# Optimization experiments

Measured on AMD Instinct MI355X. Metric: run time of the kernel, lower is better.

The kernel has to match this reference:

```python
import jax, jax.numpy as jnp
import numpy as np

NC = 80          # num_classes
REG_MAX = 16
TOPK = 10
IMG = 640
STRIDES = (8, 16, 32)
EPS = 1e-9


def make_anchors(shapes, strides):
    pts, strs = [], []
    for (h, w), s in zip(shapes, strides):
        sx = jnp.arange(w, dtype=jnp.float32)  # grid_cell_offset = 0.0
        sy = jnp.arange(h, dtype=jnp.float32)
        gy, gx = jnp.meshgrid(sy, sx, indexing='ij')
        pts.append(jnp.stack([gx, gy], -1).reshape(-1, 2))
        strs.append(jnp.full((h * w, 1), float(s), dtype=jnp.float32))
    return jnp.concatenate(pts, 0), jnp.concatenate(strs, 0)  # [A,2], [A,1]


def ciou(box1, box2, eps=1e-7):
    # boxes are xyxy, broadcastable; returns CIoU with last dim squeezed
    b1x1, b1y1, b1x2, b1y2 = jnp.split(box1, 4, -1)
    b2x1, b2y1, b2x2, b2y2 = jnp.split(box2, 4, -1)
    w1, h1 = b1x2 - b1x1, b1y2 - b1y1
    w2, h2 = b2x2 - b2x1, b2y2 - b2y1
    inter = (jnp.clip(jnp.minimum(b1x2, b2x2) - jnp.maximum(b1x1, b2x1), 0.0)
             * jnp.clip(jnp.minimum(b1y2, b2y2) - jnp.maximum(b1y1, b2y1), 0.0))
    union = w1 * h1 + w2 * h2 - inter + eps
    iou = inter / union
    cw = jnp.maximum(b1x2, b2x2) - jnp.minimum(b1x1, b2x1)
    ch = jnp.maximum(b1y2, b2y2) - jnp.minimum(b1y1, b2y1)
    c2 = cw ** 2 + ch ** 2 + eps
    rho2 = ((b2x1 + b2x2 - b1x1 - b1x2) ** 2 + (b2y1 + b2y2 - b1y1 - b1y2) ** 2) / 4.0
    v = (4.0 / np.pi ** 2) * (jnp.arctan(w2 / (h2 + eps)) - jnp.arctan(w1 / (h1 + eps))) ** 2
    alpha = jax.lax.stop_gradient(v / (v - iou + (1.0 + eps)))
    return (iou - (rho2 / c2 + v * alpha))[..., 0]


def bbox_decode(anchor_points, pred_distri):
    # distribution-focal decode: softmax over REG_MAX bins, expectation, dist2bbox
    B, A, _ = pred_distri.shape
    pd = pred_distri.reshape(B, A, 4, REG_MAX)
    proj = jnp.arange(REG_MAX, dtype=jnp.float32)
    dist = jnp.einsum('bacr,r->bac', jax.nn.softmax(pd, -1), proj)  # [B,A,4] ltrb
    lt, rb = dist[..., :2], dist[..., 2:]
    return jnp.concatenate([anchor_points - lt, anchor_points + rb], -1)  # xyxy


def assigner(pd_scores, pd_bboxes, anc_points, gt_labels, gt_bboxes, mask_gt,
             alpha=0.5, beta=6.0):
    # pd_scores [B,A,C] (sigmoid), pd_bboxes [B,A,4], gt_* [B,M,...], mask_gt [B,M,1]
    B, A, C = pd_scores.shape
    M = gt_bboxes.shape[1]
    mask_gt = mask_gt.astype(jnp.float32)
    # anchors whose center lies inside each gt box
    lt = anc_points[None, None, :, :] - gt_bboxes[:, :, None, :2]   # [B,M,A,2]
    rb = gt_bboxes[:, :, None, 2:] - anc_points[None, None, :, :]
    mask_in_gts = (jnp.minimum(lt.min(-1), rb.min(-1)) > EPS).astype(jnp.float32)  # [B,M,A]
    mask = mask_in_gts * mask_gt
    # class score of each anchor at the gt's label
    sc = jnp.take_along_axis(pd_scores[:, None, :, :],
                             gt_labels[:, :, None, None].astype(jnp.int32), axis=-1)[..., 0]  # [B,M,A]
    overlaps = jnp.clip(ciou(gt_bboxes[:, :, None, :], pd_bboxes[:, None, :, :]), 0.0) * mask
    bbox_scores = sc * mask
    align_metric = (bbox_scores ** alpha) * (overlaps ** beta)  # [B,M,A]
    # top-k candidates per gt
    _, idxs = jax.lax.top_k(align_metric, TOPK)                 # [B,M,K]
    valid = jnp.broadcast_to(mask_gt > 0, (B, M, TOPK))
    idxs = jnp.where(valid, idxs, 0)
    cnt = jnp.zeros((B * M, A), jnp.float32).at[
        jnp.arange(B * M)[:, None], idxs.reshape(B * M, TOPK)
    ].add(valid.reshape(B * M, TOPK).astype(jnp.float32)).reshape(B, M, A)
    mask_topk = jnp.where(cnt > 1, 0.0, cnt)
    mask_pos = mask_topk * mask_in_gts * mask_gt               # [B,M,A]
    # resolve anchors assigned to multiple gts by max overlap
    fg = mask_pos.sum(1)                                       # [B,A]
    multi = fg[:, None, :] > 1
    is_max = jax.nn.one_hot(overlaps.argmax(1), M, dtype=jnp.float32).transpose(0, 2, 1)
    mask_pos = jnp.where(multi, is_max, mask_pos)
    fg_mask = mask_pos.sum(1)                                  # [B,A]
    tgt_idx = mask_pos.argmax(1)                               # [B,A]
    # gather targets
    flat = tgt_idx + jnp.arange(B)[:, None] * M
    t_labels = jnp.clip(gt_labels.reshape(-1)[flat], 0)        # [B,A]
    t_bboxes = gt_bboxes.reshape(-1, 4)[flat]                  # [B,A,4]
    t_scores = jax.nn.one_hot(t_labels, C, dtype=jnp.float32) * (fg_mask[..., None] > 0)
    # normalize scores by aligned metric
    am = align_metric * mask_pos
    pos_am = am.max(-1, keepdims=True)                         # [B,M,1]
    pos_ov = (overlaps * mask_pos).max(-1, keepdims=True)      # [B,M,1]
    norm = (am * pos_ov / (pos_am + EPS)).max(1)[..., None]    # [B,A,1]
    return t_bboxes, t_scores * norm, fg_mask > 0


def setup_inputs() -> dict:
    key = jax.random.key(0)
    ks = jax.random.split(key, 9)
    B, M = 16, 32
    inp = {
        'cls0': jax.random.normal(ks[0], (B, NC, 80, 80), jnp.float32),
        'cls1': jax.random.normal(ks[1], (B, NC, 40, 40), jnp.float32),
        'cls2': jax.random.normal(ks[2], (B, NC, 20, 20), jnp.float32),
        'reg0': jax.random.normal(ks[3], (B, 4 * REG_MAX, 80, 80), jnp.float32),
        'reg1': jax.random.normal(ks[4], (B, 4 * REG_MAX, 40, 40), jnp.float32),
        'reg2': jax.random.normal(ks[5], (B, 4 * REG_MAX, 20, 20), jnp.float32),
    }
    cxy = jax.random.uniform(ks[6], (B, M, 2), minval=0.1, maxval=0.9)
    wh = jax.random.uniform(ks[7], (B, M, 2), minval=0.02, maxval=0.25)
    inp['boxes'] = jnp.concatenate([cxy, wh], -1)  # normalized cxcywh
    inp['labels'] = jax.random.randint(ks[8], (B, M), 0, NC)
    return inp


def reference(cls0, cls1, cls2, reg0, reg1, reg2, boxes, labels):
    cls_out, reg_out = [cls0, cls1, cls2], [reg0, reg1, reg2]
    B = cls0.shape[0]
    anc, stride_t = make_anchors([r.shape[2:] for r in reg_out], STRIDES)
    pred_scores = jnp.concatenate(
        [c.transpose(0, 2, 3, 1).reshape(B, -1, NC) for c in cls_out], 1)        # [B,A,C]
    pred_distri = jnp.concatenate(
        [r.transpose(0, 2, 3, 1).reshape(B, -1, 4 * REG_MAX) for r in reg_out], 1)
    # gt2xyxy: normalized cxcywh -> pixel xyxy
    cx, cy, w, h = jnp.split(boxes, 4, -1)
    gt_bboxes = jnp.concatenate([(cx - w / 2) * IMG, (cy - h / 2) * IMG,
                                 (cx + w / 2) * IMG, (cy + h / 2) * IMG], -1)
    mask_gt = gt_bboxes.sum(2, keepdims=True) > 0.0
    pred_bboxes = bbox_decode(anc, pred_distri)                                   # anchor units
    sg = jax.lax.stop_gradient
    t_bboxes, t_scores, fg_mask = assigner(
        sg(jax.nn.sigmoid(pred_scores)), sg(pred_bboxes) * stride_t,
        anc * stride_t, labels, gt_bboxes, mask_gt)
    tss = jnp.maximum(t_scores.sum(), 1.0)
    # classification BCE-with-logits
    x, t = pred_scores, t_scores
    bce = jnp.maximum(x, 0.0) - x * t + jnp.log1p(jnp.exp(-jnp.abs(x)))
    l_cls = bce.sum() / tss
    # bbox CIoU loss
    t_bboxes = t_bboxes / stride_t
    weight = t_scores.sum(-1) * fg_mask                                           # [B,A]
    iou = ciou(pred_bboxes, t_bboxes)
    l_iou = ((1.0 - iou) * weight).sum() / tss
    # DFL loss
    tltrb = jnp.clip(jnp.concatenate([anc - t_bboxes[..., :2],
                                      t_bboxes[..., 2:] - anc], -1),
                     0.0, REG_MAX - 1 - 0.01)                                     # [B,A,4]
    logp = jax.nn.log_softmax(pred_distri.reshape(B, -1, 4, REG_MAX), -1)
    tl = jnp.floor(tltrb).astype(jnp.int32)
    wl = (tl + 1).astype(jnp.float32) - tltrb
    lp_tl = jnp.take_along_axis(logp, tl[..., None], -1)[..., 0]
    lp_tr = jnp.take_along_axis(logp, (tl + 1)[..., None], -1)[..., 0]
    dfl = (-(lp_tl * wl + lp_tr * (1.0 - wl))).mean(-1)                           # [B,A]
    l_dfl = (dfl * weight).sum() / tss
    loss = jnp.stack([0.5 * l_cls, 7.5 * l_iou, 1.5 * l_dfl])
    return loss.sum(), loss
```

## Files before the change

kernel.cpp:

```cpp
#include <hip/hip_runtime.h>

#define NB 16
#define NM 32
#define NA 8400
#define NCC 80
#define NREG 64
#define A0 6400
#define A1 1600
#define A2 400
#define CAP 768

#define TILES_PER_B 34
#define DEC_BLKS (NB * TILES_PER_B)
#define ASN_BLKS (NB * NM)
#define BCE_BLKS 2048
#define MID_GRID (ASN_BLKS + BCE_BLKS)
#define PL_GRID 525


__device__ __forceinline__ void anch(int a, float& ax, float& ay, float& s, int& lvl, int& p) {
  if (a < A0)            { lvl = 0; p = a;          s = 8.f;  ax = (float)(p % 80); ay = (float)(p / 80); }
  else if (a < A0 + A1)  { lvl = 1; p = a - A0;     s = 16.f; ax = (float)(p % 40); ay = (float)(p / 40); }
  else                   { lvl = 2; p = a - A0 - A1; s = 32.f; ax = (float)(p % 20); ay = (float)(p / 20); }
}

__device__ __forceinline__ float cls_at(const float* c0, const float* c1, const float* c2,
                                        int b, int ch, int a) {
  if (a < A0)           return c0[((size_t)(b * NCC + ch)) * A0 + a];
  if (a < A0 + A1)      return c1[((size_t)(b * NCC + ch)) * A1 + (a - A0)];
  return c2[((size_t)(b * NCC + ch)) * A2 + (a - A0 - A1)];
}

__device__ __forceinline__ float reg_at(const float* r0, const float* r1, const float* r2,
                                        int b, int ch, int lvl, int p) {
  if (lvl == 0) return r0[((size_t)(b * NREG + ch)) * A0 + p];
  if (lvl == 1) return r1[((size_t)(b * NREG + ch)) * A1 + p];
  return r2[((size_t)(b * NREG + ch)) * A2 + p];
}

__device__ __forceinline__ void gtbox(const float* boxes, int b, int m,
                                      float& x1, float& y1, float& x2, float& y2, bool& valid) {
  const float* q = boxes + ((size_t)(b * NM + m)) * 4;
  float cx = q[0], cy = q[1], w = q[2], h = q[3];
  x1 = (cx - w * 0.5f) * 640.f; y1 = (cy - h * 0.5f) * 640.f;
  x2 = (cx + w * 0.5f) * 640.f; y2 = (cy + h * 0.5f) * 640.f;
  valid = (x1 + y1 + x2 + y2) > 0.f;
}

__device__ __forceinline__ float ciou_f(float b1x1, float b1y1, float b1x2, float b1y2,
                                        float b2x1, float b2y1, float b2x2, float b2y2) {
  const float eps = 1e-7f;
  float w1 = b1x2 - b1x1, h1 = b1y2 - b1y1;
  float w2 = b2x2 - b2x1, h2 = b2y2 - b2y1;
  float iw = fmaxf(fminf(b1x2, b2x2) - fmaxf(b1x1, b2x1), 0.f);
  float ih = fmaxf(fminf(b1y2, b2y2) - fmaxf(b1y1, b2y1), 0.f);
  float inter = iw * ih;
  float uni = w1 * h1 + w2 * h2 - inter + eps;
  float iou = inter / uni;
  float cw = fmaxf(b1x2, b2x2) - fminf(b1x1, b2x1);
  float ch = fmaxf(b1y2, b2y2) - fminf(b1y1, b2y1);
  float c2 = cw * cw + ch * ch + eps;
  float dx = b2x1 + b2x2 - b1x1 - b1x2;
  float dy = b2y1 + b2y2 - b1y1 - b1y2;
  float rho2 = (dx * dx + dy * dy) * 0.25f;
  float at = atanf(w2 / (h2 + eps)) - atanf(w1 / (h1 + eps));
  float v = 0.4052847345693511f * at * at;
  float alpha = v / (v - iou + (1.0f + eps));
  return iou - (rho2 / c2 + v * alpha);
}

__device__ __forceinline__ float align_of(float sc, float o) {
  float o2 = o * o, o4 = o2 * o2;
  return sqrtf(sc) * (o2 * o4);
}

__device__ __forceinline__ float softplus_fast(float x) {
  float e = __expf(-fabsf(x));
  return fmaxf(x, 0.f) + __logf(1.f + e);
}


__global__ __launch_bounds__(256) void k_dec(
    const float* r0, const float* r1, const float* r2,
    float4* bb4, float4* mls4, int* fgcnt, int* msum,
    unsigned* pos_am, unsigned* pos_ov, double* gt_acc, int* done_ctr) {
  __shared__ float lds[32 * 256];
  const int tid = threadIdx.x;
  const int g = blockIdx.x * 256 + tid;
  if (g < NB * NA) { fgcnt[g] = 0; msum[g] = 0; }
  if (g < NB * NM) { pos_am[g] = 0u; pos_ov[g] = 0u; }
  if (g < NB * NM * 4) gt_acc[g] = 0.0;
  if (g == 0) *done_ctr = 0;

  const int d = blockIdx.x;
  const int b = d / TILES_PER_B, u = d % TILES_PER_B;
  int lvl, tile;
  if (u < 25)      { lvl = 0; tile = u; }
  else if (u < 32) { lvl = 1; tile = u - 25; }
  else             { lvl = 2; tile = u - 32; }
  const int HW   = (lvl == 0) ? A0 : (lvl == 1 ? A1 : A2);
  const int W    = (lvl == 0) ? 80 : (lvl == 1 ? 40 : 20);
  const int loff = (lvl == 0) ? 0  : (lvl == 1 ? A0 : A0 + A1);
  const float* rg = (lvl == 0) ? r0 : (lvl == 1 ? r1 : r2);
  const int base_p = tile * 256;
  const int valid  = min(256, HW - base_p);
  const float* src = rg + (size_t)b * NREG * HW + base_p;

  float dist[4], mlv[4];
#pragma unroll
  for (int ph = 0; ph < 2; ++ph) {
    for (int ch = 0; ch < 32; ++ch) {
      if (tid < valid)
        lds[ch * 256 + tid] = src[(size_t)(ph * 32 + ch) * HW + tid];
    }
    __syncthreads();
    if (tid < valid) {
#pragma unroll
      for (int sh = 0; sh < 2; ++sh) {
        const float* col = &lds[(sh * 16) * 256 + tid];
        float mx = col[0];
#pragma unroll
        for (int r = 1; r < 16; ++r) mx = fmaxf(mx, col[r * 256]);
        float se = 0.f, ws = 0.f;
#pragma unroll
        for (int r = 0; r < 16; ++r) {
          float e = __expf(col[r * 256] - mx);
          se += e; ws += e * (float)r;
        }
        dist[ph * 2 + sh] = ws / se;
        mlv[ph * 2 + sh]  = mx + __logf(se);
      }
    }
    __syncthreads();
  }
  if (tid < valid) {
    int p = base_p + tid;
    float ax = (float)(p % W), ay = (float)(p / W);
    int t = b * NA + loff + p;
    bb4[t]  = make_float4(ax - dist[0], ay - dist[1], ax + dist[2], ay + dist[3]);
    mls4[t] = make_float4(mlv[0], mlv[1], mlv[2], mlv[3]);
  }
}


__global__ __launch_bounds__(256) void k_mid(
    const float* boxes, const int* labels, const float4* bb,
    const float* c0, const float* c1, const float* c2,
    int* fgcnt, int* msum, double* bce_part) {
  __shared__ float sv[CAP];
  __shared__ int   si[CAP];
  __shared__ int   s_n;
  __shared__ double sred[256];
  const int tid = threadIdx.x;

  if (blockIdx.x >= ASN_BLKS) {
    const int bce_blk = blockIdx.x - ASN_BLKS;
    const size_t N0 = (size_t)NB * NCC * A0 / 4;
    const size_t N1 = (size_t)NB * NCC * A1 / 4;
    const size_t N2 = (size_t)NB * NCC * A2 / 4;
    const size_t NT = N0 + N1 + N2;
    const float4* f0 = (const float4*)c0;
    const float4* f1 = (const float4*)c1;
    const float4* f2 = (const float4*)c2;
    const size_t i0 = (size_t)bce_blk * 256 + tid;
    const size_t stride = (size_t)BCE_BLKS * 256;
    float s0 = 0.f, s1 = 0.f;
    for (size_t i = i0; i < NT; i += stride) {
      float4 v;
      if (i < N0) v = f0[i];
      else if (i < N0 + N1) v = f1[i - N0];
      else v = f2[i - N0 - N1];
      s0 += softplus_fast(v.x) + softplus_fast(v.z);
      s1 += softplus_fast(v.y) + softplus_fast(v.w);
    }
    sred[tid] = (double)(s0 + s1);
    __syncthreads();
    for (int off = 128; off; off >>= 1) {
      if (tid < off) sred[tid] += sred[tid + off];
      __syncthreads();
    }
    if (tid == 0) bce_part[bce_blk] = sred[0];
    return;
  }

  const int bm = blockIdx.x;
  const int b = bm / NM, m = bm % NM;
  const int lane = tid & 63;

  float gx1, gy1, gx2, gy2; bool valid;
  gtbox(boxes, b, m, gx1, gy1, gx2, gy2, valid);
  if (!valid) return;
  int lbl = labels[bm]; if (lbl < 0) lbl = 0; if (lbl >= NCC) lbl = NCC - 1;
  if (tid == 0) s_n = 0;
  __syncthreads();

  const int   Ws[3]   = {80, 40, 20};
  const float ss[3]   = {8.f, 16.f, 32.f};
  const int   loff[3] = {0, A0, A0 + A1};
  int rx0[3], ry0[3], rw[3], bc[3];
  int total = 0;
  for (int l = 0; l < 3; ++l) {
    float s = ss[l]; int W = Ws[l];
    int ax0 = (int)floorf((gx1 + 1e-9f) / s);
    int ax1 = (int)ceilf((gx2 - 1e-9f) / s);
    int ay0 = (int)floorf((gy1 + 1e-9f) / s);
    int ay1 = (int)ceilf((gy2 - 1e-9f) / s);
    ax0 = max(ax0, 0); ay0 = max(ay0, 0);
    ax1 = min(ax1, W - 1); ay1 = min(ay1, W - 1);
    rx0[l] = ax0; ry0[l] = ay0;
    rw[l] = max(0, ax1 - ax0 + 1);
    int rhl = max(0, ay1 - ay0 + 1);
    bc[l] = total;
    total += rw[l] * rhl;
  }
  int iters = (total + 255) >> 8;
  for (int it = 0; it < iters; ++it) {
    int idx = it * 256 + tid;
    bool pred = false; float am = 0.f; int a = 0;
    if (idx < total) {
      int l = (idx >= bc[2]) ? 2 : ((idx >= bc[1]) ? 1 : 0);
      int r = idx - bc[l];
      int iy = r / rw[l], ix = r - iy * rw[l];
      int axg = rx0[l] + ix, ayg = ry0[l] + iy;
      a = loff[l] + ayg * Ws[l] + axg;
      float s = ss[l];
      float axp = (float)axg * s, ayp = (float)ayg * s;
      float mn = fminf(fminf(axp - gx1, ayp - gy1), fminf(gx2 - axp, gy2 - ayp));
      if (mn > 1e-9f) {
        pred = true;
        float4 pb = bb[(size_t)b * NA + a];
        float c = ciou_f(gx1, gy1, gx2, gy2, pb.x * s, pb.y * s, pb.z * s, pb.w * s);
        float o = fmaxf(c, 0.f);
        float x = cls_at(c0, c1, c2, b, lbl, a);
        float sc = 1.f / (1.f + expf(-x));
        am = align_of(sc, o);
      }
    }
    unsigned long long mask = __ballot(pred);
    if (mask) {
      int nact = __popcll(mask);
      int leader = __ffsll(mask) - 1;
      int basec = 0;
      if (lane == leader) basec = atomicAdd(&s_n, nact);
      basec = __shfl(basec, leader);
      if (pred) {
        int off = basec + __popcll(mask & ((1ull << lane) - 1ull));
        if (off < CAP) { sv[off] = am; si[off] = a; }
      }
    }
  }
  __syncthreads();
  int n = s_n; if (n > CAP) n = CAP;
  if (n == 0) return;
  if (tid >= 64) return;

  float v[12]; int ix[12];
#pragma unroll
  for (int k = 0; k < 12; ++k) {
    int j = k * 64 + tid;
    bool in = (j < n);
    v[k]  = in ? sv[j] : -2.f;
    ix[k] = in ? si[j] : (1 << 30);
  }
  int cnt = 0;
#pragma unroll
  for (int k = 0; k < 12; ++k) cnt += (v[k] > 0.f) ? 1 : 0;
  for (int o = 32; o; o >>= 1) cnt += __shfl_xor(cnt, o);
  int npos = cnt;

  if (npos > 10) {
    for (int p = 0; p < 10; ++p) {
      float bv = -1.f; int bi = 1 << 30;
#pragma unroll
      for (int k = 0; k < 12; ++k) {
        if (v[k] > bv || (v[k] == bv && ix[k] < bi)) { bv = v[k]; bi = ix[k]; }
      }
      for (int o = 32; o; o >>= 1) {
        float wv = __shfl_xor(bv, o); int wi = __shfl_xor(bi, o);
        if (wv > bv || (wv == bv && wi < bi)) { bv = wv; bi = wi; }
      }
#pragma unroll
      for (int k = 0; k < 12; ++k) if (ix[k] == bi) v[k] = -1.f;
      if (tid == 0) {
        atomicAdd(&fgcnt[(size_t)b * NA + bi], 1);
        atomicAdd(&msum[(size_t)b * NA + bi], m);
      }
    }
  } else {
#pragma unroll
    for (int k = 0; k < 12; ++k) {
      if (v[k] > 0.f) {
        atomicAdd(&fgcnt[(size_t)b * NA + ix[k]], 1);
        atomicAdd(&msum[(size_t)b * NA + ix[k]], m);
      }
    }
    int need = 10 - npos;
    for (int j = tid; j < n; j += 64) {
      if (sv[j] == 0.f) {
        int i = si[j];
        if (i < 10) {
          int pb = 0;
          for (int q = 0; q < n; ++q) pb += (sv[q] > 0.f && si[q] < i) ? 1 : 0;
          if (i - pb < need) {
            atomicAdd(&fgcnt[(size_t)b * NA + i], 1);
            atomicAdd(&msum[(size_t)b * NA + i], m);
          }
        }
      }
    }
  }
}


__global__ __launch_bounds__(256) void k_rpf(
    const float* boxes, const int* labels,
    const float4* bb, const float4* mls,
    const float* c0, const float* c1, const float* c2,
    const float* r0, const float* r1, const float* r2,
    const int* fgcnt, const int* msum,
    unsigned* pos_am, unsigned* pos_ov, double* gt_acc,
    int* done_ctr, const double* bce_part, float* out) {
  const int tid = threadIdx.x;
  const int t = blockIdx.x * 256 + tid;
  int fg = fgcnt[t];
  if (fg > 0) {
    int b = t / NA, a = t % NA;
    float ax, ay, s; int lvl, p;
    anch(a, ax, ay, s, lvl, p);
    float axp = ax * s, ayp = ay * s;
    float4 pb = bb[t];
    float px1 = pb.x * s, py1 = pb.y * s, px2 = pb.z * s, py2 = pb.w * s;
    int asn; float o;
    if (fg == 1) {
      asn = msum[t];
      float gx1, gy1, gx2, gy2; bool valid;
      gtbox(boxes, b, asn, gx1, gy1, gx2, gy2, valid);
      o = fmaxf(ciou_f(gx1, gy1, gx2, gy2, px1, py1, px2, py2), 0.f);
    } else {
      float bv = -1e30f; int bi = 0;
      for (int m = 0; m < NM; ++m) {
        float gx1, gy1, gx2, gy2; bool valid;
        gtbox(boxes, b, m, gx1, gy1, gx2, gy2, valid);
        float om = 0.f;
        if (valid) {
          float mn = fminf(fminf(axp - gx1, ayp - gy1), fminf(gx2 - axp, gy2 - ayp));
          if (mn > 1e-9f)
            om = fmaxf(ciou_f(gx1, gy1, gx2, gy2, px1, py1, px2, py2), 0.f);
        }
        if (om > bv) { bv = om; bi = m; }
      }
      asn = bi; o = bv;
    }
    if (o > 0.f) {
      int g = b * NM + asn;
      int lbl = labels[g]; if (lbl < 0) lbl = 0; if (lbl >= NCC) lbl = NCC - 1;
      float x = cls_at(c0, c1, c2, b, lbl, a);
      float sc = 1.f / (1.f + expf(-x));
      float am = align_of(sc, o);
      atomicMax(&pos_am[g], __float_as_uint(am));
      atomicMax(&pos_ov[g], __float_as_uint(o));
      if (am > 0.f) {
        float gx1, gy1, gx2, gy2; bool valid;
        gtbox(boxes, b, asn, gx1, gy1, gx2, gy2, valid);
        float inv_s = 1.f / s;
        float tx1 = gx1 * inv_s, ty1 = gy1 * inv_s, tx2 = gx2 * inv_s, ty2 = gy2 * inv_s;
        float iou = ciou_f(pb.x, pb.y, pb.z, pb.w, tx1, ty1, tx2, ty2);
        float4 ml = mls[t];
        float tgt[4] = { ax - tx1, ay - ty1, tx2 - ax, ty2 - ay };
        float mlv[4] = { ml.x, ml.y, ml.z, ml.w };
        float dfl = 0.f;
        for (int sd = 0; sd < 4; ++sd) {
          float tv = fminf(fmaxf(tgt[sd], 0.f), 14.99f);
          float tlf = floorf(tv);
          int tl = (int)tlf;
          float wl = (tlf + 1.f) - tv;
          float xtl = reg_at(r0, r1, r2, b, sd * 16 + tl,     lvl, p);
          float xtr = reg_at(r0, r1, r2, b, sd * 16 + tl + 1, lvl, p);
          dfl += -((xtl - mlv[sd]) * wl + (xtr - mlv[sd]) * (1.f - wl));
        }
        dfl *= 0.25f;
        atomicAdd(&gt_acc[g * 4 + 0], (double)am);
        atomicAdd(&gt_acc[g * 4 + 1], (double)(am * x));
        atomicAdd(&gt_acc[g * 4 + 2], (double)(am * (1.f - iou)));
        atomicAdd(&gt_acc[g * 4 + 3], (double)(am * dfl));
      }
    }
  }

  __shared__ int s_last;
  __syncthreads();
  if (tid == 0) {
    int old = atomicAdd(done_ctr, 1);
    s_last = (old == (int)gridDim.x - 1) ? 1 : 0;
  }
  __syncthreads();
  if (!s_last) return;

  double tss = 0.0, sx = 0.0, siou = 0.0, sdfl = 0.0, bce = 0.0;
  for (int g = tid; g < NB * NM; g += 256) {
    float pam = __uint_as_float(atomicAdd(&pos_am[g], 0u));
    float pov = __uint_as_float(atomicAdd(&pos_ov[g], 0u));
    double sc = (double)pov / ((double)pam + 1e-9);
    tss  += atomicAdd(&gt_acc[g * 4 + 0], 0.0) * sc;
    sx   += atomicAdd(&gt_acc[g * 4 + 1], 0.0) * sc;
    siou += atomicAdd(&gt_acc[g * 4 + 2], 0.0) * sc;
    sdfl += atomicAdd(&gt_acc[g * 4 + 3], 0.0) * sc;
  }
  for (int i = tid; i < BCE_BLKS; i += 256) bce += bce_part[i];
  __shared__ double sred[256];
  double vals[5] = { tss, sx, siou, sdfl, bce };
  double tot[5];
  for (int q = 0; q < 5; ++q) {
    sred[tid] = vals[q];
    __syncthreads();
    for (int off = 128; off; off >>= 1) {
      if (tid < off) sred[tid] += sred[tid + off];
      __syncthreads();
    }
    tot[q] = sred[0];
    __syncthreads();
  }
  if (tid == 0) {
    double t5 = tot[0]; if (t5 < 1.0) t5 = 1.0;
    double l0 = 0.5 * (tot[4] - tot[1]) / t5;
    double l1 = 7.5 * tot[2] / t5;
    double l2 = 1.5 * tot[3] / t5;
    out[0] = (float)(l0 + l1 + l2);
    out[1] = (float)l0;
    out[2] = (float)l1;
    out[3] = (float)l2;
  }
}


extern "C" void kernel_launch(void* const* d_in, const int* in_sizes, int n_in,
                              void* d_out, int out_size, void* d_ws, size_t ws_size,
                              hipStream_t stream) {
  (void)in_sizes; (void)n_in; (void)out_size; (void)ws_size;
  const float* cls0  = (const float*)d_in[0];
  const float* cls1  = (const float*)d_in[1];
  const float* cls2  = (const float*)d_in[2];
  const float* reg0  = (const float*)d_in[3];
  const float* reg1  = (const float*)d_in[4];
  const float* reg2  = (const float*)d_in[5];
  const float* boxes = (const float*)d_in[6];
  const int*   labels = (const int*)d_in[7];
  float* out = (float*)d_out;

  const size_t BA = (size_t)NB * NA;
  const int    BM = NB * NM;

  char* wsb = (char*)d_ws;
  double*   bce_part = (double*)wsb;
  double*   gt_acc   = bce_part + BCE_BLKS;
  unsigned* pos_am   = (unsigned*)(gt_acc + (size_t)BM * 4);
  unsigned* pos_ov   = pos_am + BM;
  int*      done_ctr = (int*)(pos_ov + BM);
  int*      fgcnt    = done_ctr + 4;
  int*      msum     = fgcnt + BA;
  float*    bbp      = (float*)(msum + BA);
  float*    mlsp     = bbp + BA * 4;

  float4* bb  = (float4*)bbp;
  float4* mls = (float4*)mlsp;

  k_dec<<<DEC_BLKS, 256, 0, stream>>>(reg0, reg1, reg2, bb, mls,
                                      fgcnt, msum, pos_am, pos_ov, gt_acc, done_ctr);
  k_mid<<<MID_GRID, 256, 0, stream>>>(boxes, labels, (const float4*)bb,
                                      cls0, cls1, cls2, fgcnt, msum, bce_part);
  k_rpf<<<PL_GRID, 256, 0, stream>>>(boxes, labels, (const float4*)bb, (const float4*)mls,
                                     cls0, cls1, cls2, reg0, reg1, reg2,
                                     fgcnt, msum, pos_am, pos_ov, gt_acc,
                                     done_ctr, bce_part, out);
}
```

Measured before the change: 58.62 us.

## Split BCE reduction across decode and assign kernels; vectorize regression loads

The BCE softplus reduction over the class logits is split in half. One half now runs in extra blocks appended to the decode kernel, and the other half stays alongside the assigner blocks. Those extra decode-kernel blocks also take over zeroing the workspace. The aim is to spread the large class-logit read across two launches so it overlaps with the lighter decode and assign work. Separately, the decode kernel now loads regression logits into LDS with float4 loads instead of scalar loads, to cut the number of load instructions; this relies on every level's row length and tile offset being a multiple of four floats.

```diff
diff --git a/kernel.cpp b/kernel.cpp
--- a/kernel.cpp
+++ b/kernel.cpp
@@ -13,8 +13,10 @@
 #define TILES_PER_B 34
 #define DEC_BLKS (NB * TILES_PER_B)
 #define ASN_BLKS (NB * NM)
-#define BCE_BLKS 2048
-#define MID_GRID (ASN_BLKS + BCE_BLKS)
+#define BCE1_BLKS 1024
+#define BCE2_BLKS 1024
+#define G1 (DEC_BLKS + BCE1_BLKS)
+#define G2 (ASN_BLKS + BCE2_BLKS)
 #define PL_GRID 525
 
 
@@ -79,18 +81,56 @@
   return fmaxf(x, 0.f) + __logf(1.f + e);
 }
 
-
-__global__ __launch_bounds__(256) void k_dec(
+__device__ __forceinline__ void bce_range(const float* c0, const float* c1, const float* c2,
+                                          int blk, int nblk, size_t lo, size_t hi,
+                                          double* slot, double* sred, int tid) {
+  const size_t N0 = (size_t)NB * NCC * A0 / 4;
+  const size_t N1 = (size_t)NB * NCC * A1 / 4;
+  const float4* f0 = (const float4*)c0;
+  const float4* f1 = (const float4*)c1;
+  const float4* f2 = (const float4*)c2;
+  float s0 = 0.f, s1 = 0.f;
+  for (size_t i = lo + (size_t)blk * 256 + tid; i < hi; i += (size_t)nblk * 256) {
+    float4 v;
+    if (i < N0) v = f0[i];
+    else if (i < N0 + N1) v = f1[i - N0];
+    else v = f2[i - N0 - N1];
+    s0 += softplus_fast(v.x) + softplus_fast(v.z);
+    s1 += softplus_fast(v.y) + softplus_fast(v.w);
+  }
+  sred[tid] = (double)(s0 + s1);
+  __syncthreads();
+  for (int off = 128; off; off >>= 1) {
+    if (tid < off) sred[tid] += sred[tid + off];
+    __syncthreads();
+  }
+  if (tid == 0) *slot = sred[0];
+}
+
+#define NT4 ((size_t)NB * NCC * NA / 4)
+#define NT4_HALF (NT4 / 2)
+
+
+__global__ __launch_bounds__(256) void k_d1(
     const float* r0, const float* r1, const float* r2,
+    const float* c0, const float* c1, const float* c2,
     float4* bb4, float4* mls4, int* fgcnt, int* msum,
-    unsigned* pos_am, unsigned* pos_ov, double* gt_acc, int* done_ctr) {
-  __shared__ float lds[32 * 256];
+    unsigned* pos_am, unsigned* pos_ov, double* gt_acc, int* done_ctr,
+    double* bce_part) {
+  __shared__ __align__(16) float lds[32 * 256];
   const int tid = threadIdx.x;
-  const int g = blockIdx.x * 256 + tid;
-  if (g < NB * NA) { fgcnt[g] = 0; msum[g] = 0; }
-  if (g < NB * NM) { pos_am[g] = 0u; pos_ov[g] = 0u; }
-  if (g < NB * NM * 4) gt_acc[g] = 0.0;
-  if (g == 0) *done_ctr = 0;
+
+  if (blockIdx.x >= DEC_BLKS) {
+    const int zb = blockIdx.x - DEC_BLKS;
+    const int gz = zb * 256 + tid;
+    if (gz < NB * NA) { fgcnt[gz] = 0; msum[gz] = 0; }
+    if (gz < NB * NM) { pos_am[gz] = 0u; pos_ov[gz] = 0u; }
+    if (gz < NB * NM * 4) gt_acc[gz] = 0.0;
+    if (gz == 0) *done_ctr = 0;
+    bce_range(c0, c1, c2, zb, BCE1_BLKS, 0, NT4_HALF,
+              &bce_part[zb], (double*)lds, tid);
+    return;
+  }
 
   const int d = blockIdx.x;
   const int b = d / TILES_PER_B, u = d % TILES_PER_B;
@@ -106,12 +146,19 @@
   const int valid  = min(256, HW - base_p);
   const float* src = rg + (size_t)b * NREG * HW + base_p;
 
+  const int g4 = tid >> 6;
+  const int l4 = tid & 63;
+
   float dist[4], mlv[4];
 #pragma unroll
   for (int ph = 0; ph < 2; ++ph) {
-    for (int ch = 0; ch < 32; ++ch) {
-      if (tid < valid)
-        lds[ch * 256 + tid] = src[(size_t)(ph * 32 + ch) * HW + tid];
+    if (l4 * 4 < valid) {
+#pragma unroll
+      for (int c4 = 0; c4 < 8; ++c4) {
+        int ch = c4 * 4 + g4;
+        float4 v = *(const float4*)(src + (size_t)(ph * 32 + ch) * HW + l4 * 4);
+        *(float4*)&lds[ch * 256 + l4 * 4] = v;
+      }
     }
     __syncthreads();
     if (tid < valid) {
@@ -143,7 +190,7 @@
 }
 
 
-__global__ __launch_bounds__(256) void k_mid(
+__global__ __launch_bounds__(256) void k_d2(
     const float* boxes, const int* labels, const float4* bb,
     const float* c0, const float* c1, const float* c2,
     int* fgcnt, int* msum, double* bce_part) {
@@ -154,32 +201,9 @@
   const int tid = threadIdx.x;
 
   if (blockIdx.x >= ASN_BLKS) {
-    const int bce_blk = blockIdx.x - ASN_BLKS;
-    const size_t N0 = (size_t)NB * NCC * A0 / 4;
-    const size_t N1 = (size_t)NB * NCC * A1 / 4;
-    const size_t N2 = (size_t)NB * NCC * A2 / 4;
-    const size_t NT = N0 + N1 + N2;
-    const float4* f0 = (const float4*)c0;
-    const float4* f1 = (const float4*)c1;
-    const float4* f2 = (const float4*)c2;
-    const size_t i0 = (size_t)bce_blk * 256 + tid;
-    const size_t stride = (size_t)BCE_BLKS * 256;
-    float s0 = 0.f, s1 = 0.f;
-    for (size_t i = i0; i < NT; i += stride) {
-      float4 v;
-      if (i < N0) v = f0[i];
-      else if (i < N0 + N1) v = f1[i - N0];
-      else v = f2[i - N0 - N1];
-      s0 += softplus_fast(v.x) + softplus_fast(v.z);
-      s1 += softplus_fast(v.y) + softplus_fast(v.w);
-    }
-    sred[tid] = (double)(s0 + s1);
-    __syncthreads();
-    for (int off = 128; off; off >>= 1) {
-      if (tid < off) sred[tid] += sred[tid + off];
-      __syncthreads();
-    }
-    if (tid == 0) bce_part[bce_blk] = sred[0];
+    const int zb = blockIdx.x - ASN_BLKS;
+    bce_range(c0, c1, c2, zb, BCE2_BLKS, NT4_HALF, NT4,
+              &bce_part[BCE1_BLKS + zb], sred, tid);
     return;
   }
 
@@ -406,7 +430,7 @@
     siou += atomicAdd(&gt_acc[g * 4 + 2], 0.0) * sc;
     sdfl += atomicAdd(&gt_acc[g * 4 + 3], 0.0) * sc;
   }
-  for (int i = tid; i < BCE_BLKS; i += 256) bce += bce_part[i];
+  for (int i = tid; i < BCE1_BLKS + BCE2_BLKS; i += 256) bce += bce_part[i];
   __shared__ double sred[256];
   double vals[5] = { tss, sx, siou, sdfl, bce };
   double tot[5];
@@ -452,7 +476,7 @@
 
   char* wsb = (char*)d_ws;
   double*   bce_part = (double*)wsb;
-  double*   gt_acc   = bce_part + BCE_BLKS;
+  double*   gt_acc   = bce_part + BCE1_BLKS + BCE2_BLKS;
   unsigned* pos_am   = (unsigned*)(gt_acc + (size_t)BM * 4);
   unsigned* pos_ov   = pos_am + BM;
   int*      done_ctr = (int*)(pos_ov + BM);
@@ -464,10 +488,10 @@
   float4* bb  = (float4*)bbp;
   float4* mls = (float4*)mlsp;
 
-  k_dec<<<DEC_BLKS, 256, 0, stream>>>(reg0, reg1, reg2, bb, mls,
-                                      fgcnt, msum, pos_am, pos_ov, gt_acc, done_ctr);
-  k_mid<<<MID_GRID, 256, 0, stream>>>(boxes, labels, (const float4*)bb,
-                                      cls0, cls1, cls2, fgcnt, msum, bce_part);
+  k_d1<<<G1, 256, 0, stream>>>(reg0, reg1, reg2, cls0, cls1, cls2, bb, mls,
+                               fgcnt, msum, pos_am, pos_ov, gt_acc, done_ctr, bce_part);
+  k_d2<<<G2, 256, 0, stream>>>(boxes, labels, (const float4*)bb,
+                               cls0, cls1, cls2, fgcnt, msum, bce_part);
   k_rpf<<<PL_GRID, 256, 0, stream>>>(boxes, labels, (const float4*)bb, (const float4*)mls,
                                      cls0, cls1, cls2, reg0, reg1, reg2,
                                      fgcnt, msum, pos_am, pos_ov, gt_acc,
```

Result: slower. 60.50 us (+3.2%).
